# Kernel optimization log

Measured on AMD Instinct MI355X. Metric: run time of the kernel, lower is better.

## Reference

```python
import jax, jax.numpy as jnp
import numpy as np

TEMP = 0.7
EPS = 1e-6
LN_EPS = 1e-5
CAP_FACTOR = 2.0


def setup_inputs() -> dict:
    key = jax.random.key(0)
    B, S, H, E = 8, 4096, 2048, 8
    H2 = H // 2
    ks = jax.random.split(key, 3)
    x = jax.random.normal(ks[0], (B, S, H), jnp.float32)
    ln_w = jnp.ones((H,), jnp.float32)
    ln_b = jnp.zeros((H,), jnp.float32)
    # kaiming_normal_(fan_in, relu): std = sqrt(2 / fan_in)
    w1 = jax.random.normal(ks[1], (H2, H), jnp.float32) * np.float32(np.sqrt(2.0 / H))
    b1 = jnp.zeros((H2,), jnp.float32)
    w2 = jax.random.normal(ks[2], (E, H2), jnp.float32) * np.float32(np.sqrt(2.0 / H2))
    b2 = jnp.zeros((E,), jnp.float32)
    return {"x": x, "ln_w": ln_w, "ln_b": ln_b, "w1": w1, "b1": b1,
            "w2": w2, "b2": b2, "top_k": 2, "num_experts": E}


def _forward(x, ln_w, ln_b, w1, b1, w2, b2, top_k, num_experts):
    B, S, H = x.shape
    N = B * S
    # router: LayerNorm -> Linear -> GELU(exact) -> Linear
    mu = x.mean(-1, keepdims=True)
    var = jnp.mean((x - mu) ** 2, axis=-1, keepdims=True)
    h = (x - mu) * jax.lax.rsqrt(var + LN_EPS) * ln_w + ln_b
    h = jax.nn.gelu(h @ w1.T + b1, approximate=False)
    logits = h @ w2.T + b2
    ew = jnp.clip(logits / TEMP, -50.0, 50.0)  # [B,S,E]

    flat = ew.reshape(N, num_experts)
    capacity = int(CAP_FACTOR * N * top_k / num_experts)

    # top-k per token + softmax over the k selected logits, scatter into dense mask
    tk_w, tk_i = jax.lax.top_k(flat, top_k)          # [N,k]
    sm = jax.nn.softmax(tk_w, axis=-1)               # [N,k]
    rows = jnp.arange(N)[:, None]
    masks = jnp.zeros((N, num_experts), flat.dtype).at[rows, tk_i].set(sm)

    # capacity drop: per expert column, if sum of weights > capacity keep only
    # the top-`capacity` weighted tokens (extra zero-valued picks are no-ops,
    # matching the torch min(capacity, nnz) behavior).
    cols = masks.T                                   # [E,N]
    sums = cols.sum(-1)                              # [E]
    kcap = min(capacity, N)
    tv, ti = jax.lax.top_k(cols, kcap)               # [E,kcap]
    erow = jnp.arange(num_experts)[:, None]
    capped = jnp.zeros_like(cols).at[erow, ti].set(tv)
    over = sums > capacity
    cols = jnp.where(over[:, None], capped, cols)
    count = jax.lax.stop_gradient(jnp.where(over, capped.sum(-1), sums))  # buffer, no grad

    masks = cols.T
    masks = masks / jnp.maximum(masks.sum(-1, keepdims=True), EPS)

    usage = count / jnp.maximum(count.sum(), EPS)
    target = jnp.full((num_experts,), 1.0 / num_experts, usage.dtype)
    # F.kl_div(log(usage), target, reduction='batchmean') with batch dim = E
    kl = jnp.sum(target * (jnp.log(target) - jnp.log(jnp.maximum(usage, EPS)))) / num_experts
    loss = 0.01 * kl
    return ew, masks.reshape(B, S, num_experts), loss, usage


def reference(x, ln_w, ln_b, w1, b1, w2, b2, top_k, num_experts):
    return _forward(x, ln_w, ln_b, w1, b1, w2, b2, top_k, num_experts)
```

## Files before the change

kernel.cpp:

```cpp
#include <hip/hip_runtime.h>
#include <math.h>

#define NTOK 32768
#define HDIM 2048
#define H2DIM 1024
#define NE 8

#define WS_LOGITS 0
#define WS_SUMS 262144
#define WS_C1 262160
#define WS_C2 263184
#define WS_W1_BYTES 1057024ull
#define WS_NEED (WS_W1_BYTES + 8388608ull)

#define OUT_MASKS 262144
#define OUT_LOSS 524288
#define OUT_USAGE 524289

typedef _Float16 half8 __attribute__((ext_vector_type(8)));
typedef float floatx16 __attribute__((ext_vector_type(16)));

#define H_SCALE 0.03125f

__global__ __launch_bounds__(256) void w1prep_kernel(
    const float* __restrict__ w1, const float* __restrict__ ln_w,
    const float* __restrict__ ln_b, _Float16* __restrict__ w1p,
    float* __restrict__ ws) {
  const int tid = threadIdx.x;
  ((float4*)(ws + WS_LOGITS))[blockIdx.x * 256 + tid] =
      make_float4(0.f, 0.f, 0.f, 0.f);
  if (blockIdx.x == 0 && tid < NE) ws[WS_SUMS + tid] = 0.f;

  const int n = blockIdx.x * 4 + (tid >> 6);
  const int kc = tid & 63;
  const float4* src = (const float4*)(w1 + (size_t)n * HDIM + kc * 32);
  const float4* lwp = (const float4*)(ln_w + kc * 32);
  const float4* lbp = (const float4*)(ln_b + kc * 32);
  float wv[32], lwv[32], lbv[32];
#pragma unroll
  for (int v = 0; v < 8; ++v) {
    float4 f = src[v], g = lwp[v], h = lbp[v];
    wv[v*4+0]=f.x; wv[v*4+1]=f.y; wv[v*4+2]=f.z; wv[v*4+3]=f.w;
    lwv[v*4+0]=g.x; lwv[v*4+1]=g.y; lwv[v*4+2]=g.z; lwv[v*4+3]=g.w;
    lbv[v*4+0]=h.x; lbv[v*4+1]=h.y; lbv[v*4+2]=h.z; lbv[v*4+3]=h.w;
  }
  float c1 = 0.f, c2 = 0.f;
  _Float16 hi[32], lo[32];
#pragma unroll
  for (int v = 0; v < 32; ++v) {
    float wp = wv[v] * lwv[v];
    c1 += wp;
    c2 += lbv[v] * wv[v];
    float t = wp * 32.0f;
    hi[v] = (_Float16)t;
    lo[v] = (_Float16)((t - (float)hi[v]) * 4096.0f);
  }
  _Float16* dst = w1p + ((size_t)(n >> 5) * 64 + kc) * 2048;
  const int ln8 = (n & 31) * 8;
#pragma unroll
  for (int st = 0; st < 2; ++st)
#pragma unroll
    for (int f = 0; f < 2; ++f) {
      const int b = st * 16 + f * 8;
      half8 h = {hi[b+0],hi[b+1],hi[b+2],hi[b+3],hi[b+4],hi[b+5],hi[b+6],hi[b+7]};
      half8 l = {lo[b+0],lo[b+1],lo[b+2],lo[b+3],lo[b+4],lo[b+5],lo[b+6],lo[b+7]};
      *(half8*)&dst[st * 1024 + 0 + f * 256 + ln8] = h;
      *(half8*)&dst[st * 1024 + 512 + f * 256 + ln8] = l;
    }
#pragma unroll
  for (int o = 1; o < 64; o <<= 1) {
    c1 += __shfl_xor(c1, o);
    c2 += __shfl_xor(c2, o);
  }
  if (kc == 0) {
    ws[WS_C1 + n] = c1;
    ws[WS_C2 + n] = c2;
  }
}

#define LDST(P, ks)                                                  \
  P##a00 = *(const float4*)(pa0 + (size_t)(ks) * 16);                \
  P##a01 = *(const float4*)(pa0 + (size_t)(ks) * 16 + 4);            \
  P##a10 = *(const float4*)(pa1 + (size_t)(ks) * 16);                \
  P##a11 = *(const float4*)(pa1 + (size_t)(ks) * 16 + 4);            \
  P##bh0 = *(const half8*)(pb0 + (size_t)(ks) * 1024);               \
  P##bl0 = *(const half8*)(pb0 + (size_t)(ks) * 1024 + 512);         \
  P##bh1 = *(const half8*)(pb1 + (size_t)(ks) * 1024);               \
  P##bl1 = *(const half8*)(pb1 + (size_t)(ks) * 1024 + 512);

#define STEP(P)                                                               \
  {                                                                           \
    float f0[8] = {P##a00.x, P##a00.y, P##a00.z, P##a00.w,                    \
                   P##a01.x, P##a01.y, P##a01.z, P##a01.w};                   \
    float f1[8] = {P##a10.x, P##a10.y, P##a10.z, P##a10.w,                    \
                   P##a11.x, P##a11.y, P##a11.z, P##a11.w};                   \
    half8 ah0, al0, ah1, al1;                                                 \
    _Pragma("unroll") for (int v = 0; v < 8; ++v) {                           \
      sA[0] += f0[v]; sqA[0] = fmaf(f0[v], f0[v], sqA[0]);                    \
      sA[1] += f1[v]; sqA[1] = fmaf(f1[v], f1[v], sqA[1]);                    \
      ah0[v] = (_Float16)f0[v];                                               \
      al0[v] = (_Float16)((f0[v] - (float)ah0[v]) * 4096.0f);                 \
      ah1[v] = (_Float16)f1[v];                                               \
      al1[v] = (_Float16)((f1[v] - (float)ah1[v]) * 4096.0f);                 \
    }                                                                         \
    __builtin_amdgcn_s_setprio(1);                                            \
    acc[0][0] = __builtin_amdgcn_mfma_f32_32x32x16_f16(ah0, P##bh0, acc[0][0], 0, 0, 0);   \
    accL[0][0] = __builtin_amdgcn_mfma_f32_32x32x16_f16(ah0, P##bl0, accL[0][0], 0, 0, 0); \
    accL[0][0] = __builtin_amdgcn_mfma_f32_32x32x16_f16(al0, P##bh0, accL[0][0], 0, 0, 0); \
    acc[0][1] = __builtin_amdgcn_mfma_f32_32x32x16_f16(ah0, P##bh1, acc[0][1], 0, 0, 0);   \
    accL[0][1] = __builtin_amdgcn_mfma_f32_32x32x16_f16(ah0, P##bl1, accL[0][1], 0, 0, 0); \
    accL[0][1] = __builtin_amdgcn_mfma_f32_32x32x16_f16(al0, P##bh1, accL[0][1], 0, 0, 0); \
    acc[1][0] = __builtin_amdgcn_mfma_f32_32x32x16_f16(ah1, P##bh0, acc[1][0], 0, 0, 0);   \
    accL[1][0] = __builtin_amdgcn_mfma_f32_32x32x16_f16(ah1, P##bl0, accL[1][0], 0, 0, 0); \
    accL[1][0] = __builtin_amdgcn_mfma_f32_32x32x16_f16(al1, P##bh0, accL[1][0], 0, 0, 0); \
    acc[1][1] = __builtin_amdgcn_mfma_f32_32x32x16_f16(ah1, P##bh1, acc[1][1], 0, 0, 0);   \
    accL[1][1] = __builtin_amdgcn_mfma_f32_32x32x16_f16(ah1, P##bl1, accL[1][1], 0, 0, 0); \
    accL[1][1] = __builtin_amdgcn_mfma_f32_32x32x16_f16(al1, P##bh1, accL[1][1], 0, 0, 0); \
    __builtin_amdgcn_s_setprio(0);                                            \
  }

__global__ __launch_bounds__(256, 2) void gemm_mfma_kernel(
    const float* __restrict__ x, const _Float16* __restrict__ w1p,
    const float* __restrict__ bias1, const float* __restrict__ w2,
    const float* __restrict__ C1, const float* __restrict__ C2,
    float* __restrict__ logits) {
  const int tid = threadIdx.x;
  const int lin = blockIdx.x;
  const int xcd = lin & 7, jj = lin >> 3;
  const int m0 = (xcd * 32 + (jj >> 3)) * 128;
  const int n0 = (jj & 7) * 128;

  const int lane = tid & 63;
  const int wid = tid >> 6;
  const int wm = wid >> 1, wn = wid & 1;
  const int fr = lane & 31, fq = lane >> 5;

  const float* pa0 = x + (size_t)(m0 + wm * 64 + fr) * HDIM + fq * 8;
  const float* pa1 = pa0 + (size_t)32 * HDIM;
  const _Float16* pb0 =
      w1p + ((size_t)((n0 >> 5) + wn * 2) * 64) * 2048 + lane * 8;
  const _Float16* pb1 = pb0 + (size_t)64 * 2048;

  floatx16 acc[2][2], accL[2][2];
#pragma unroll
  for (int i = 0; i < 2; ++i)
#pragma unroll
    for (int j = 0; j < 2; ++j)
#pragma unroll
      for (int r = 0; r < 16; ++r) {
        acc[i][j][r] = 0.f;
        accL[i][j][r] = 0.f;
      }
  float sA[2] = {0.f, 0.f}, sqA[2] = {0.f, 0.f};

  float4 Ea00, Ea01, Ea10, Ea11, Oa00, Oa01, Oa10, Oa11;
  half8 Ebh0, Ebl0, Ebh1, Ebl1, Obh0, Obl0, Obh1, Obl1;

  LDST(E, 0);
  for (int ks = 0; ks < 128; ks += 2) {
    LDST(O, ks + 1);
    STEP(E);
    if (ks < 126) { LDST(E, ks + 2); }
    STEP(O);
  }

  sA[0] += __shfl_xor(sA[0], 32);
  sqA[0] += __shfl_xor(sqA[0], 32);
  sA[1] += __shfl_xor(sA[1], 32);
  sqA[1] += __shfl_xor(sqA[1], 32);

  const float inv_sqrt2 = 0.70710678118654752440f;
  const int c = fr;
  const int col0 = n0 + wn * 64 + c;
  const int col1 = col0 + 32;
  float w2r0[NE], w2r1[NE];
#pragma unroll
  for (int e = 0; e < NE; ++e) {
    w2r0[e] = w2[e * H2DIM + col0];
    w2r1[e] = w2[e * H2DIM + col1];
  }
  const float c1a = C1[col0], c1b = C1[col1];
  const float hb0 = C2[col0] + bias1[col0];
  const float hb1 = C2[col1] + bias1[col1];

#pragma unroll
  for (int i = 0; i < 2; ++i)
#pragma unroll
    for (int r = 0; r < 16; ++r) {
      const int rr = (r & 3) + 8 * (r >> 2) + 4 * fq;
      const float srow = __shfl(sA[i], rr);
      const float sqrow = __shfl(sqA[i], rr);
      const float mu_r = srow * (1.0f / HDIM);
      const float var = fmaxf(sqrow * (1.0f / HDIM) - mu_r * mu_r, 0.0f);
      const float rsr = 1.0f / sqrtf(var + 1e-5f);
      const float nmr = -rsr * mu_r;
      const float a0 = fmaf(accL[i][0][r], (1.0f / 4096.0f), acc[i][0][r]);
      const float a1 = fmaf(accL[i][1][r], (1.0f / 4096.0f), acc[i][1][r]);
      float h0 = fmaf(a0 * H_SCALE, rsr, fmaf(nmr, c1a, hb0));
      float h1 = fmaf(a1 * H_SCALE, rsr, fmaf(nmr, c1b, hb1));
      float g0 = 0.5f * h0 * (1.0f + erff(h0 * inv_sqrt2));
      float g1 = 0.5f * h1 * (1.0f + erff(h1 * inv_sqrt2));
      float pl[NE];
#pragma unroll
      for (int e = 0; e < NE; ++e) pl[e] = fmaf(g0, w2r0[e], g1 * w2r1[e]);
#pragma unroll
      for (int o = 1; o <= 16; o <<= 1)
#pragma unroll
        for (int e = 0; e < NE; ++e) pl[e] += __shfl_xor(pl[e], o);
      if (c == 0) {
        const int row = m0 + wm * 64 + i * 32 + rr;
#pragma unroll
        for (int e = 0; e < NE; ++e)
          atomicAdd(&logits[(size_t)row * NE + e], pl[e]);
      }
    }
}

__global__ __launch_bounds__(256) void route_kernel(const float* __restrict__ logits,
                                                    const float* __restrict__ b2,
                                                    float* __restrict__ out,
                                                    float* __restrict__ sums) {
  __shared__ float ssum[NE];
  if (threadIdx.x < NE) ssum[threadIdx.x] = 0.f;
  __syncthreads();

  int tok = blockIdx.x * 256 + threadIdx.x;
  const float4* lp = (const float4*)(logits + (size_t)tok * NE);
  float4 l0 = lp[0], l1 = lp[1];
  float lv[NE] = {l0.x, l0.y, l0.z, l0.w, l1.x, l1.y, l1.z, l1.w};
  float ew[NE];
#pragma unroll
  for (int e = 0; e < NE; ++e) {
    float v = (lv[e] + b2[e]) / 0.7f;
    ew[e] = fminf(fmaxf(v, -50.0f), 50.0f);
  }

  int i1 = 0;
  float v1 = ew[0];
#pragma unroll
  for (int e = 1; e < NE; ++e)
    if (ew[e] > v1) { v1 = ew[e]; i1 = e; }
  int i2 = -1;
  float v2 = -1e30f;
#pragma unroll
  for (int e = 0; e < NE; ++e)
    if (e != i1 && ew[e] > v2) { v2 = ew[e]; i2 = e; }

  float t = expf(v2 - v1);
  float sm1 = 1.0f / (1.0f + t);
  float sm2 = t / (1.0f + t);
  float rsum = fmaxf(sm1 + sm2, 1e-6f);
  float m1 = sm1 / rsum, m2 = sm2 / rsum;

  float4* oew = (float4*)(out + (size_t)tok * NE);
  oew[0] = make_float4(ew[0], ew[1], ew[2], ew[3]);
  oew[1] = make_float4(ew[4], ew[5], ew[6], ew[7]);

  float mv[NE];
#pragma unroll
  for (int e = 0; e < NE; ++e)
    mv[e] = (e == i1) ? m1 : ((e == i2) ? m2 : 0.0f);
  float4* om = (float4*)(out + OUT_MASKS + (size_t)tok * NE);
  om[0] = make_float4(mv[0], mv[1], mv[2], mv[3]);
  om[1] = make_float4(mv[4], mv[5], mv[6], mv[7]);

  atomicAdd(&ssum[i1], sm1);
  atomicAdd(&ssum[i2], sm2);
  __syncthreads();
  if (threadIdx.x < NE) atomicAdd(&sums[threadIdx.x], ssum[threadIdx.x]);
}

__global__ void finalize_kernel(const float* __restrict__ sums,
                                float* __restrict__ out) {
  if (threadIdx.x != 0 || blockIdx.x != 0) return;
  float c[NE], tot = 0.f;
  for (int e = 0; e < NE; ++e) {
    c[e] = sums[e];
    tot += c[e];
  }
  float target = 1.0f / NE;
  float lt = logf(target);
  float kl = 0.f;
  for (int e = 0; e < NE; ++e) {
    float u = c[e] / fmaxf(tot, 1e-6f);
    out[OUT_USAGE + e] = u;
    kl += target * (lt - logf(fmaxf(u, 1e-6f)));
  }
  out[OUT_LOSS] = 0.01f * (kl / NE);
}

extern "C" void kernel_launch(void* const* d_in, const int* in_sizes, int n_in,
                              void* d_out, int out_size, void* d_ws, size_t ws_size,
                              hipStream_t stream) {
  const float* x = (const float*)d_in[0];
  const float* ln_w = (const float*)d_in[1];
  const float* ln_b = (const float*)d_in[2];
  const float* w1 = (const float*)d_in[3];
  const float* b1 = (const float*)d_in[4];
  const float* w2 = (const float*)d_in[5];
  const float* b2 = (const float*)d_in[6];
  float* out = (float*)d_out;
  float* ws = (float*)d_ws;
  _Float16* w1p = (_Float16*)((char*)d_ws + WS_W1_BYTES);
  (void)ws_size;

  w1prep_kernel<<<256, 256, 0, stream>>>(w1, ln_w, ln_b, w1p, ws);
  gemm_mfma_kernel<<<2048, 256, 0, stream>>>(
      x, w1p, b1, w2, ws + WS_C1, ws + WS_C2, ws + WS_LOGITS);
  route_kernel<<<NTOK / 256, 256, 0, stream>>>(ws + WS_LOGITS, b2, out,
                                               ws + WS_SUMS);
  finalize_kernel<<<1, 64, 0, stream>>>(ws + WS_SUMS, out);
}
```

Measured before the change: 1.148 ms.

## Stage GEMM operands through LDS ring via direct global-to-LDS loads, precompute row stats

Replaces the register double-buffered global loads in the GEMM main loop with a 4-deep LDS ring filled by global_load_lds, using swizzled offsets and waitcnt/barrier-based pipelining. LayerNorm row sums and sums of squares move out of the GEMM inner loop into a separate pass in the prep kernel. The stats are stashed temporarily in the masks region of the output and later overwritten. The x matrix is now read twice (once for stats, once for the GEMM), and every k-step adds a block barrier.

```diff
diff --git a/kernel.cpp b/kernel.cpp
--- a/kernel.cpp
+++ b/kernel.cpp
@@ -11,7 +11,6 @@
 #define WS_C1 262160
 #define WS_C2 263184
 #define WS_W1_BYTES 1057024ull
-#define WS_NEED (WS_W1_BYTES + 8388608ull)
 
 #define OUT_MASKS 262144
 #define OUT_LOSS 524288
@@ -22,11 +21,45 @@
 
 #define H_SCALE 0.03125f
 
-__global__ __launch_bounds__(256) void w1prep_kernel(
+#define GLDS16(g, l)                                                   \
+  __builtin_amdgcn_global_load_lds(                                    \
+      (const __attribute__((address_space(1))) void*)(g),              \
+      (__attribute__((address_space(3))) void*)(l), 16, 0, 0)
+
+__global__ __launch_bounds__(256) void prep_kernel(
     const float* __restrict__ w1, const float* __restrict__ ln_w,
-    const float* __restrict__ ln_b, _Float16* __restrict__ w1p,
-    float* __restrict__ ws) {
+    const float* __restrict__ ln_b, const float* __restrict__ x,
+    _Float16* __restrict__ w1p, float* __restrict__ ws,
+    float* __restrict__ srow, float* __restrict__ sqrow) {
   const int tid = threadIdx.x;
+  const int lane = tid & 63;
+
+  {
+    const int n = blockIdx.x * 4 + (tid >> 6);
+    const float4* p = (const float4*)(x + (size_t)n * HDIM);
+    float s = 0.f, sq = 0.f;
+#pragma unroll
+    for (int v = 0; v < 8; ++v) {
+      float4 f = p[lane + v * 64];
+      s += f.x + f.y + f.z + f.w;
+      sq = fmaf(f.x, f.x, sq);
+      sq = fmaf(f.y, f.y, sq);
+      sq = fmaf(f.z, f.z, sq);
+      sq = fmaf(f.w, f.w, sq);
+    }
+#pragma unroll
+    for (int o = 1; o < 64; o <<= 1) {
+      s += __shfl_xor(s, o);
+      sq += __shfl_xor(sq, o);
+    }
+    if (lane == 0) {
+      srow[n] = s;
+      sqrow[n] = sq;
+    }
+  }
+
+  if (blockIdx.x >= 256) return;
+
   ((float4*)(ws + WS_LOGITS))[blockIdx.x * 256 + tid] =
       make_float4(0.f, 0.f, 0.f, 0.f);
   if (blockIdx.x == 0 && tid < NE) ws[WS_SUMS + tid] = 0.f;
@@ -78,44 +111,57 @@
   }
 }
 
-#define LDST(P, ks)                                                  \
-  P##a00 = *(const float4*)(pa0 + (size_t)(ks) * 16);                \
-  P##a01 = *(const float4*)(pa0 + (size_t)(ks) * 16 + 4);            \
-  P##a10 = *(const float4*)(pa1 + (size_t)(ks) * 16);                \
-  P##a11 = *(const float4*)(pa1 + (size_t)(ks) * 16 + 4);            \
-  P##bh0 = *(const half8*)(pb0 + (size_t)(ks) * 1024);               \
-  P##bl0 = *(const half8*)(pb0 + (size_t)(ks) * 1024 + 512);         \
-  P##bh1 = *(const half8*)(pb1 + (size_t)(ks) * 1024);               \
-  P##bl1 = *(const half8*)(pb1 + (size_t)(ks) * 1024 + 512);
-
-#define STEP(P)                                                               \
+#define STAGE(h)                                                              \
   {                                                                           \
-    float f0[8] = {P##a00.x, P##a00.y, P##a00.z, P##a00.w,                    \
-                   P##a01.x, P##a01.y, P##a01.z, P##a01.w};                   \
-    float f1[8] = {P##a10.x, P##a10.y, P##a10.z, P##a10.w,                    \
-                   P##a11.x, P##a11.y, P##a11.z, P##a11.w};                   \
+    char* sp = ringc + (((h) & 3) * 16384);                                   \
+    GLDS16(aS0 + (size_t)(h) * 64, sp + (2 * wid) * 1024);                    \
+    GLDS16(aS1 + (size_t)(h) * 64, sp + (2 * wid + 1) * 1024);                \
+    GLDS16(bS0 + (size_t)(h) * 2048, sp + 8192 + wid * 2048);                 \
+    GLDS16(bS1 + (size_t)(h) * 2048, sp + 8192 + wid * 2048 + 1024);          \
+  }
+
+#define CVTI(f0, f1, ah, al)                                                  \
+  {                                                                           \
+    float xa[8] = {f0.x, f0.y, f0.z, f0.w, f1.x, f1.y, f1.z, f1.w};           \
+    _Pragma("unroll") for (int v = 0; v < 8; ++v) {                           \
+      ah[v] = (_Float16)xa[v];                                                \
+      al[v] = (_Float16)((xa[v] - (float)ah[v]) * 4096.0f);                   \
+    }                                                                         \
+  }
+
+#define STEPBODY(h, VM, DOSTAGE)                                              \
+  {                                                                           \
+    asm volatile("s_waitcnt vmcnt(" #VM ")" ::: "memory");                    \
+    __builtin_amdgcn_s_barrier();                                             \
+    __builtin_amdgcn_sched_barrier(0);                                        \
+    if (DOSTAGE) STAGE((h) + 3);                                              \
+    __builtin_amdgcn_sched_barrier(0);                                        \
+    const char* As = ringc + ((h) & 3) * 16384;                               \
+    const char* Bs = As + 8192;                                               \
+    float4 a00 = *(const float4*)(As + aof00);                                \
+    float4 a01 = *(const float4*)(As + aof01);                                \
+    float4 a10 = *(const float4*)(As + aof10);                                \
+    float4 a11 = *(const float4*)(As + aof11);                                \
+    half8 bh0 = *(const half8*)(Bs + bof0);                                   \
+    half8 bl0 = *(const half8*)(Bs + bof0 + 1024);                            \
+    half8 bh1 = *(const half8*)(Bs + bof1);                                   \
+    half8 bl1 = *(const half8*)(Bs + bof1 + 1024);                            \
     half8 ah0, al0, ah1, al1;                                                 \
-    _Pragma("unroll") for (int v = 0; v < 8; ++v) {                           \
-      sA[0] += f0[v]; sqA[0] = fmaf(f0[v], f0[v], sqA[0]);                    \
-      sA[1] += f1[v]; sqA[1] = fmaf(f1[v], f1[v], sqA[1]);                    \
-      ah0[v] = (_Float16)f0[v];                                               \
-      al0[v] = (_Float16)((f0[v] - (float)ah0[v]) * 4096.0f);                 \
-      ah1[v] = (_Float16)f1[v];                                               \
-      al1[v] = (_Float16)((f1[v] - (float)ah1[v]) * 4096.0f);                 \
-    }                                                                         \
+    CVTI(a00, a01, ah0, al0);                                                 \
+    CVTI(a10, a11, ah1, al1);                                                 \
     __builtin_amdgcn_s_setprio(1);                                            \
-    acc[0][0] = __builtin_amdgcn_mfma_f32_32x32x16_f16(ah0, P##bh0, acc[0][0], 0, 0, 0);   \
-    accL[0][0] = __builtin_amdgcn_mfma_f32_32x32x16_f16(ah0, P##bl0, accL[0][0], 0, 0, 0); \
-    accL[0][0] = __builtin_amdgcn_mfma_f32_32x32x16_f16(al0, P##bh0, accL[0][0], 0, 0, 0); \
-    acc[0][1] = __builtin_amdgcn_mfma_f32_32x32x16_f16(ah0, P##bh1, acc[0][1], 0, 0, 0);   \
-    accL[0][1] = __builtin_amdgcn_mfma_f32_32x32x16_f16(ah0, P##bl1, accL[0][1], 0, 0, 0); \
-    accL[0][1] = __builtin_amdgcn_mfma_f32_32x32x16_f16(al0, P##bh1, accL[0][1], 0, 0, 0); \
-    acc[1][0] = __builtin_amdgcn_mfma_f32_32x32x16_f16(ah1, P##bh0, acc[1][0], 0, 0, 0);   \
-    accL[1][0] = __builtin_amdgcn_mfma_f32_32x32x16_f16(ah1, P##bl0, accL[1][0], 0, 0, 0); \
-    accL[1][0] = __builtin_amdgcn_mfma_f32_32x32x16_f16(al1, P##bh0, accL[1][0], 0, 0, 0); \
-    acc[1][1] = __builtin_amdgcn_mfma_f32_32x32x16_f16(ah1, P##bh1, acc[1][1], 0, 0, 0);   \
-    accL[1][1] = __builtin_amdgcn_mfma_f32_32x32x16_f16(ah1, P##bl1, accL[1][1], 0, 0, 0); \
-    accL[1][1] = __builtin_amdgcn_mfma_f32_32x32x16_f16(al1, P##bh1, accL[1][1], 0, 0, 0); \
+    acc[0][0] = __builtin_amdgcn_mfma_f32_32x32x16_f16(ah0, bh0, acc[0][0], 0, 0, 0);   \
+    accL[0][0] = __builtin_amdgcn_mfma_f32_32x32x16_f16(ah0, bl0, accL[0][0], 0, 0, 0); \
+    accL[0][0] = __builtin_amdgcn_mfma_f32_32x32x16_f16(al0, bh0, accL[0][0], 0, 0, 0); \
+    acc[0][1] = __builtin_amdgcn_mfma_f32_32x32x16_f16(ah0, bh1, acc[0][1], 0, 0, 0);   \
+    accL[0][1] = __builtin_amdgcn_mfma_f32_32x32x16_f16(ah0, bl1, accL[0][1], 0, 0, 0); \
+    accL[0][1] = __builtin_amdgcn_mfma_f32_32x32x16_f16(al0, bh1, accL[0][1], 0, 0, 0); \
+    acc[1][0] = __builtin_amdgcn_mfma_f32_32x32x16_f16(ah1, bh0, acc[1][0], 0, 0, 0);   \
+    accL[1][0] = __builtin_amdgcn_mfma_f32_32x32x16_f16(ah1, bl0, accL[1][0], 0, 0, 0); \
+    accL[1][0] = __builtin_amdgcn_mfma_f32_32x32x16_f16(al1, bh0, accL[1][0], 0, 0, 0); \
+    acc[1][1] = __builtin_amdgcn_mfma_f32_32x32x16_f16(ah1, bh1, acc[1][1], 0, 0, 0);   \
+    accL[1][1] = __builtin_amdgcn_mfma_f32_32x32x16_f16(ah1, bl1, accL[1][1], 0, 0, 0); \
+    accL[1][1] = __builtin_amdgcn_mfma_f32_32x32x16_f16(al1, bh1, accL[1][1], 0, 0, 0); \
     __builtin_amdgcn_s_setprio(0);                                            \
   }
 
@@ -123,7 +169,11 @@
     const float* __restrict__ x, const _Float16* __restrict__ w1p,
     const float* __restrict__ bias1, const float* __restrict__ w2,
     const float* __restrict__ C1, const float* __restrict__ C2,
+    const float* __restrict__ srow, const float* __restrict__ sqrow,
     float* __restrict__ logits) {
+  __shared__ __align__(16) char ring[4][16384];
+  __shared__ float sRowL[128], sqRowL[128];
+
   const int tid = threadIdx.x;
   const int lin = blockIdx.x;
   const int xcd = lin & 7, jj = lin >> 3;
@@ -135,11 +185,27 @@
   const int wm = wid >> 1, wn = wid & 1;
   const int fr = lane & 31, fq = lane >> 5;
 
-  const float* pa0 = x + (size_t)(m0 + wm * 64 + fr) * HDIM + fq * 8;
-  const float* pa1 = pa0 + (size_t)32 * HDIM;
-  const _Float16* pb0 =
-      w1p + ((size_t)((n0 >> 5) + wn * 2) * 64) * 2048 + lane * 8;
-  const _Float16* pb1 = pb0 + (size_t)64 * 2048;
+  if (tid < 128) {
+    sRowL[tid] = srow[m0 + tid];
+    sqRowL[tid] = sqrow[m0 + tid];
+  }
+
+  const char* aS0 = (const char*)x +
+      (size_t)(m0 + 32 * wid + (lane >> 2)) * (HDIM * 4) +
+      (((lane & 3) ^ ((lane >> 3) & 3)) << 4);
+  const char* aS1 = aS0 + (size_t)16 * (HDIM * 4);
+  const char* bS0 = (const char*)w1p +
+      (size_t)((n0 >> 5) + wid) * 64 * 4096 + lane * 16;
+  const char* bS1 = bS0 + 1024;
+  char* ringc = &ring[0][0];
+
+  const int sw = (fr >> 1) & 3;
+  const int aof00 = (64 * wm + fr) * 64 + ((((fq << 1) | 0) ^ sw) << 4);
+  const int aof01 = (64 * wm + fr) * 64 + ((((fq << 1) | 1) ^ sw) << 4);
+  const int aof10 = (64 * wm + 32 + fr) * 64 + ((((fq << 1) | 0) ^ sw) << 4);
+  const int aof11 = (64 * wm + 32 + fr) * 64 + ((((fq << 1) | 1) ^ sw) << 4);
+  const int bof0 = (2 * wn) * 2048 + lane * 16;
+  const int bof1 = (2 * wn + 1) * 2048 + lane * 16;
 
   floatx16 acc[2][2], accL[2][2];
 #pragma unroll
@@ -151,23 +217,18 @@
         acc[i][j][r] = 0.f;
         accL[i][j][r] = 0.f;
       }
-  float sA[2] = {0.f, 0.f}, sqA[2] = {0.f, 0.f};
-
-  float4 Ea00, Ea01, Ea10, Ea11, Oa00, Oa01, Oa10, Oa11;
-  half8 Ebh0, Ebl0, Ebh1, Ebl1, Obh0, Obl0, Obh1, Obl1;
-
-  LDST(E, 0);
-  for (int ks = 0; ks < 128; ks += 2) {
-    LDST(O, ks + 1);
-    STEP(E);
-    if (ks < 126) { LDST(E, ks + 2); }
-    STEP(O);
-  }
-
-  sA[0] += __shfl_xor(sA[0], 32);
-  sqA[0] += __shfl_xor(sqA[0], 32);
-  sA[1] += __shfl_xor(sA[1], 32);
-  sqA[1] += __shfl_xor(sqA[1], 32);
+
+  STAGE(0);
+  STAGE(1);
+  STAGE(2);
+
+#pragma unroll 1
+  for (int hs = 0; hs < 125; ++hs) {
+    STEPBODY(hs, 8, 1);
+  }
+  STEPBODY(125, 8, 0);
+  STEPBODY(126, 4, 0);
+  STEPBODY(127, 0, 0);
 
   const float inv_sqrt2 = 0.70710678118654752440f;
   const int c = fr;
@@ -187,11 +248,10 @@
   for (int i = 0; i < 2; ++i)
 #pragma unroll
     for (int r = 0; r < 16; ++r) {
-      const int rr = (r & 3) + 8 * (r >> 2) + 4 * fq;
-      const float srow = __shfl(sA[i], rr);
-      const float sqrow = __shfl(sqA[i], rr);
-      const float mu_r = srow * (1.0f / HDIM);
-      const float var = fmaxf(sqrow * (1.0f / HDIM) - mu_r * mu_r, 0.0f);
+      const int lr = wm * 64 + i * 32 + (r & 3) + 8 * (r >> 2) + 4 * fq;
+      const float mu_r = sRowL[lr] * (1.0f / HDIM);
+      const float var =
+          fmaxf(sqRowL[lr] * (1.0f / HDIM) - mu_r * mu_r, 0.0f);
       const float rsr = 1.0f / sqrtf(var + 1e-5f);
       const float nmr = -rsr * mu_r;
       const float a0 = fmaf(accL[i][0][r], (1.0f / 4096.0f), acc[i][0][r]);
@@ -208,7 +268,7 @@
 #pragma unroll
         for (int e = 0; e < NE; ++e) pl[e] += __shfl_xor(pl[e], o);
       if (c == 0) {
-        const int row = m0 + wm * 64 + i * 32 + rr;
+        const int row = m0 + lr;
 #pragma unroll
         for (int e = 0; e < NE; ++e)
           atomicAdd(&logits[(size_t)row * NE + e], pl[e]);
@@ -304,9 +364,12 @@
   _Float16* w1p = (_Float16*)((char*)d_ws + WS_W1_BYTES);
   (void)ws_size;
 
-  w1prep_kernel<<<256, 256, 0, stream>>>(w1, ln_w, ln_b, w1p, ws);
+  float* srow = out + OUT_MASKS;
+  float* sqrow = out + OUT_MASKS + NTOK;
+
+  prep_kernel<<<8192, 256, 0, stream>>>(w1, ln_w, ln_b, x, w1p, ws, srow, sqrow);
   gemm_mfma_kernel<<<2048, 256, 0, stream>>>(
-      x, w1p, b1, w2, ws + WS_C1, ws + WS_C2, ws + WS_LOGITS);
+      x, w1p, b1, w2, ws + WS_C1, ws + WS_C2, srow, sqrow, ws + WS_LOGITS);
   route_kernel<<<NTOK / 256, 256, 0, stream>>>(ws + WS_LOGITS, b2, out,
                                                ws + WS_SUMS);
   finalize_kernel<<<1, 64, 0, stream>>>(ws + WS_SUMS, out);
```

After: 1.267 ms. +10.4%, slower.
